# Performance work log

Hardware: AMD Instinct MI355X
Metric: run time of the kernel (lower is better)

## Reference

```python
import jax, jax.numpy as jnp
import numpy as np

N_NODES = 50000
N_EDGES = 800000
IN_CH = 128
HEADS = 4
OUT_CH = 4
N_GRAPHS = 64
NEG_SLOPE = 0.2  # GATv2Conv default leaky_relu slope
EPS = 1e-5       # GraphNorm eps


def _seg_sum(x, seg, n):
    return jax.ops.segment_sum(x, seg, num_segments=n)


def _seg_mean(x, seg, n):
    s = _seg_sum(x, seg, n)
    cnt = _seg_sum(jnp.ones((seg.shape[0],), x.dtype), seg, n)
    return s / jnp.maximum(cnt, 1.0)[:, None]


def gatv2_conv(x, src, dst, n, w_l, w_r, att, bias, heads, out_ch, concat):
    # x: [N, F_in]; src/dst: [E_tot] (self-loops already appended)
    x_l = (x @ w_l).reshape(n, heads, out_ch)
    x_r = (x @ w_r).reshape(n, heads, out_ch)
    m = jax.nn.leaky_relu(x_l[src] + x_r[dst], NEG_SLOPE)   # [E, H, C]
    e = jnp.einsum('ehc,hc->eh', m, att)                    # [E, H]
    # softmax over incoming edges of each destination node
    e_max = jax.ops.segment_max(e, dst, num_segments=n)     # [N, H]
    w = jnp.exp(e - e_max[dst])
    denom = _seg_sum(w, dst, n)                             # [N, H]
    alpha = w / denom[dst]
    out = _seg_sum(alpha[:, :, None] * x_l[src], dst, n)    # [N, H, C]
    out = out.reshape(n, heads * out_ch) if concat else out.mean(axis=1)
    return out + bias


def graph_norm(x, batch, weight, bias, mean_scale, n_graphs):
    mu = _seg_mean(x, batch, n_graphs)                      # [G, C]
    out = x - mu[batch] * mean_scale
    var = _seg_mean(out * out, batch, n_graphs)
    return out / jnp.sqrt(var[batch] + EPS) * weight + bias


def setup_inputs() -> dict:
    key = jax.random.key(0)
    ks = jax.random.split(key, 20)
    H = HEADS
    d = {}
    d['x'] = jax.random.normal(ks[0], (N_NODES, IN_CH), dtype=jnp.float32)
    d['edge_index'] = jax.random.randint(ks[1], (2, N_EDGES), 0, N_NODES, dtype=jnp.int32)
    d['batch'] = jnp.sort(jax.random.randint(ks[2], (N_NODES,), 0, N_GRAPHS, dtype=jnp.int32))
    def glorot(k, shape):
        fan = shape[0] + shape[-1]
        return jax.random.normal(k, shape, dtype=jnp.float32) * np.sqrt(2.0 / fan).astype(np.float32)
    # layer 1: in 128 -> 32 per head, concat -> 128
    d['w_l1'] = glorot(ks[3], (IN_CH, H * 32)); d['w_r1'] = glorot(ks[4], (IN_CH, H * 32))
    d['att1'] = glorot(ks[5], (H, 32)); d['b1'] = jnp.zeros((H * 32,), jnp.float32)
    d['gn1_w'] = jnp.ones((H * 32,), jnp.float32); d['gn1_b'] = jnp.zeros((H * 32,), jnp.float32); d['gn1_s'] = jnp.ones((H * 32,), jnp.float32)
    # layer 2: 128 -> 16 per head, concat -> 64
    d['w_l2'] = glorot(ks[6], (H * 32, H * 16)); d['w_r2'] = glorot(ks[7], (H * 32, H * 16))
    d['att2'] = glorot(ks[8], (H, 16)); d['b2'] = jnp.zeros((H * 16,), jnp.float32)
    d['gn2_w'] = jnp.ones((H * 16,), jnp.float32); d['gn2_b'] = jnp.zeros((H * 16,), jnp.float32); d['gn2_s'] = jnp.ones((H * 16,), jnp.float32)
    # layer 3: 64 -> 8 per head, mean over heads -> 8
    d['w_l3'] = glorot(ks[9], (H * 16, H * 8)); d['w_r3'] = glorot(ks[10], (H * 16, H * 8))
    d['att3'] = glorot(ks[11], (H, 8)); d['b3'] = jnp.zeros((8,), jnp.float32)
    d['gn3_w'] = jnp.ones((8,), jnp.float32); d['gn3_b'] = jnp.zeros((8,), jnp.float32); d['gn3_s'] = jnp.ones((8,), jnp.float32)
    d['lin_w'] = glorot(ks[12], (8, OUT_CH)); d['lin_b'] = jnp.zeros((OUT_CH,), jnp.float32)
    return d


def reference(x, edge_index, batch,
              w_l1, w_r1, att1, b1, gn1_w, gn1_b, gn1_s,
              w_l2, w_r2, att2, b2, gn2_w, gn2_b, gn2_s,
              w_l3, w_r3, att3, b3, gn3_w, gn3_b, gn3_s,
              lin_w, lin_b):
    n = x.shape[0]
    loop = jnp.arange(n, dtype=edge_index.dtype)
    src = jnp.concatenate([edge_index[0], loop])  # add_self_loops=True (PyG default)
    dst = jnp.concatenate([edge_index[1], loop])
    h = gatv2_conv(x, src, dst, n, w_l1, w_r1, att1, b1, HEADS, 32, True)
    h = jax.nn.relu(graph_norm(h, batch, gn1_w, gn1_b, gn1_s, N_GRAPHS))
    h = gatv2_conv(h, src, dst, n, w_l2, w_r2, att2, b2, HEADS, 16, True)
    h = jax.nn.relu(graph_norm(h, batch, gn2_w, gn2_b, gn2_s, N_GRAPHS))
    h = gatv2_conv(h, src, dst, n, w_l3, w_r3, att3, b3, HEADS, 8, False)
    h = jax.nn.relu(graph_norm(h, batch, gn3_w, gn3_b, gn3_s, N_GRAPHS))
    features = _seg_mean(h, batch, N_GRAPHS)  # global_mean_pool -> [G, 8]
    logits = features @ lin_w + lin_b         # [G, OUT_CH]
    return (logits, features)
```

## Files before the change

### kernel.cpp

```cpp
#include <hip/hip_runtime.h>
#include <hip/hip_fp16.h>
#include <math.h>

#define NN 50000
#define NE 800000
#define ET (NE + NN)
#define NG 64
#define H 4
#define NBK 196
#define CH 2048
#define SB ((ET + CH - 1) / CH)
#define GD ((NN + 63) / 64)

typedef _Float16 half8 __attribute__((ext_vector_type(8)));
typedef _Float16 half4 __attribute__((ext_vector_type(4)));
typedef _Float16 hv2 __attribute__((ext_vector_type(2)));
typedef float floatx4 __attribute__((ext_vector_type(4)));


template <int K, int M2>
__device__ __forceinline__ void wprep_fn(int chunk, const float* __restrict__ Wl, const float* __restrict__ Wr,
                                         _Float16* __restrict__ Wfrag) {
    constexpr int MTOT = 2 * M2, NT = MTOT / 16;
    if (chunk >= MTOT * K / 8) return;
    int lane = chunk & 63, tt = chunk >> 6;
    int t = tt % NT, kt = tt / NT;
    int n = t * 16 + (lane & 15);
    int kb = kt * 32 + (lane >> 4) * 8;
    const float* src = (n < M2) ? (Wl + n) : (Wr + (n - M2));
    half8 h;
#pragma unroll
    for (int j = 0; j < 8; ++j) h[j] = (_Float16)src[(size_t)(kb + j) * M2];
    *(half8*)(Wfrag + (size_t)chunk * 8) = h;
}


__global__ __launch_bounds__(256) void k_prep(const float* __restrict__ Wl1, const float* __restrict__ Wr1,
                                              const float* __restrict__ Wl2, const float* __restrict__ Wr2,
                                              const float* __restrict__ Wl3, const float* __restrict__ Wr3,
                                              _Float16* __restrict__ Wf1, _Float16* __restrict__ Wf2,
                                              _Float16* __restrict__ Wf3,
                                              const int* __restrict__ batch, int* __restrict__ bpos,
                                              const int* __restrict__ ei, int* __restrict__ bcnt) {
    int b = blockIdx.x, t = threadIdx.x;
    if (b < 16) { wprep_fn<128, 128>(b * 256 + t, Wl1, Wr1, Wf1); return; }
    if (b < 24) { wprep_fn<128, 64>((b - 16) * 256 + t, Wl2, Wr2, Wf2); return; }
    if (b < 26) { wprep_fn<64, 32>((b - 24) * 256 + t, Wl3, Wr3, Wf3); return; }
    if (b < 26 + NBK) {
        int i = (b - 26) * 256 + t;
        if (i >= NN) return;
        int cur = batch[i];
        int prev = (i == 0) ? -1 : batch[i - 1];
        for (int g = prev + 1; g <= cur; ++g) bpos[g] = i;
        if (i == NN - 1)
            for (int g = cur + 1; g <= NG; ++g) bpos[g] = NN;
        return;
    }
    __shared__ int hist[NBK];
    int b0 = b - 26 - NBK;
    for (int i = t; i < NBK; i += 256) hist[i] = 0;
    __syncthreads();
#pragma unroll
    for (int pass = 0; pass < CH / 256; ++pass) {
        int e = b0 * CH + pass * 256 + t;
        if (e < ET) {
            int d = (e < NE) ? ei[NE + e] : (e - NE);
            atomicAdd(&hist[d >> 8], 1);
        }
    }
    __syncthreads();
    if (t < NBK) bcnt[t * SB + b0] = hist[t];
}


template <typename AT, bool NORM>
__device__ __forceinline__ half8 load_a8(const AT* __restrict__ ap, const float* pa, const float* pb) {
    if constexpr (NORM) {
        half8 raw = *(const half8*)ap;
        half8 h;
#pragma unroll
        for (int j = 0; j < 8; ++j) {
            float y = fmaf((float)raw[j], pa[j], pb[j]);
            h[j] = (_Float16)fmaxf(y, 0.f);
        }
        return h;
    } else if constexpr (__is_same(AT, _Float16)) {
        return *(const half8*)ap;
    } else {
        const float4* p = (const float4*)ap;
        float4 a = p[0], b = p[1];
        half8 h;
        h[0] = (_Float16)a.x; h[1] = (_Float16)a.y; h[2] = (_Float16)a.z; h[3] = (_Float16)a.w;
        h[4] = (_Float16)b.x; h[5] = (_Float16)b.y; h[6] = (_Float16)b.z; h[7] = (_Float16)b.w;
        return h;
    }
}

template <int K, int M2, typename AT, bool NORM>
__device__ __forceinline__ void dualgemm_body(int blk, int tid, const AT* __restrict__ Ain,
                                              const _Float16* __restrict__ Wfrag,
                                              __half* __restrict__ Ol, __half* __restrict__ Or,
                                              const float* __restrict__ gsum, const float* __restrict__ gsq,
                                              const float* __restrict__ gw, const float* __restrict__ gbb,
                                              const float* __restrict__ gms,
                                              const int* __restrict__ bpos, const int* __restrict__ batch) {
    constexpr int MTOT = 2 * M2;
    constexpr int NT = MTOT / 16;
    constexpr int KT = K / 32;
    constexpr int PK = NORM ? K : 1;
    __shared__ float spab[2][8][PK];
    int wid = tid >> 6, lane = tid & 63;
    int q = lane >> 4, l15 = lane & 15;
    int r0 = blk * 64 + wid * 16;
    int arow = min(r0 + l15, NN - 1);
    const AT* ap = Ain + (size_t)arow * K + q * 8;
    const float *pa = nullptr, *pb = nullptr;
    if constexpr (NORM) {
        int rb = blk * 64;
        int g0 = batch[min(rb, NN - 1)];
        int g1 = batch[min(rb + 63, NN - 1)];
        int gspan = min(g1 - g0 + 1, 8);
        for (int i = tid; i < gspan * K; i += 256) {
            int gg = i / K, c = i - gg * K;
            int g = g0 + gg;
            float cg = fmaxf((float)(bpos[g + 1] - bpos[g]), 1.f);
            float mu = gsum[(size_t)g * K + c] / cg;
            float ex2 = gsq[(size_t)g * K + c] / cg;
            float s_ = gms[c];
            float var = ex2 - s_ * (2.f - s_) * mu * mu;
            float a = rsqrtf(var + 1e-5f) * gw[c];
            spab[0][gg][c] = a;
            spab[1][gg][c] = gbb[c] - mu * s_ * a;
        }
        __syncthreads();
        int gg = min(batch[arow] - g0, 7);
        pa = &spab[0][gg][q * 8];
        pb = &spab[1][gg][q * 8];
    }

    floatx4 acc[NT];
#pragma unroll
    for (int t = 0; t < NT; ++t) acc[t] = (floatx4){0.f, 0.f, 0.f, 0.f};

#pragma unroll
    for (int kt = 0; kt < KT; ++kt) {
        half8 a8 = load_a8<AT, NORM>(ap + kt * 32, pa + (NORM ? kt * 32 : 0), pb + (NORM ? kt * 32 : 0));
        const _Float16* wp = Wfrag + ((size_t)(kt * NT) * 64 + lane) * 8;
#pragma unroll
        for (int t = 0; t < NT; ++t) {
            half8 b8 = *(const half8*)(wp + (size_t)t * 64 * 8);
            acc[t] = __builtin_amdgcn_mfma_f32_16x16x32_f16(a8, b8, acc[t], 0, 0, 0);
        }
    }

#pragma unroll
    for (int t = 0; t < NT; ++t) {
        int cn = t * 16 + l15;
#pragma unroll
        for (int reg = 0; reg < 4; ++reg) {
            int r = r0 + q * 4 + reg;
            if (r < NN) {
                if (cn < M2) Ol[(size_t)r * M2 + cn] = __float2half(acc[t][reg]);
                else         Or[(size_t)r * M2 + (cn - M2)] = __float2half(acc[t][reg]);
            }
        }
    }
}

template <int K, int M2>
__global__ __launch_bounds__(256) void k_dualgemm_n(const __half* __restrict__ Ain,
                                                    const _Float16* __restrict__ Wfrag,
                                                    __half* __restrict__ Ol, __half* __restrict__ Or,
                                                    const float* __restrict__ gsum, const float* __restrict__ gsq,
                                                    const float* __restrict__ gw, const float* __restrict__ gbb,
                                                    const float* __restrict__ gms,
                                                    const int* __restrict__ bpos, const int* __restrict__ batch) {
    dualgemm_body<K, M2, _Float16, true>(blockIdx.x, threadIdx.x, (const _Float16*)Ain, Wfrag, Ol, Or,
                                         gsum, gsq, gw, gbb, gms, bpos, batch);
}


__device__ __forceinline__ void bscanA_fn(int b, int t, const int* __restrict__ bcnt,
                                          int* __restrict__ boff, int* __restrict__ tot) {
    __shared__ int lds[256];
    int i0 = 2 * t, i1 = 2 * t + 1;
    int v0 = (i0 < SB) ? bcnt[b * SB + i0] : 0;
    int v1 = (i1 < SB) ? bcnt[b * SB + i1] : 0;
    int pair = v0 + v1;
    lds[t] = pair;
    __syncthreads();
    for (int off = 1; off < 256; off <<= 1) {
        int y = (t >= off) ? lds[t - off] : 0;
        __syncthreads();
        lds[t] += y;
        __syncthreads();
    }
    int excl = lds[t] - pair;
    if (i0 < SB) boff[b * SB + i0] = excl;
    if (i1 < SB) boff[b * SB + i1] = excl + v0;
    if (t == 255) tot[b] = lds[255];
}


__global__ __launch_bounds__(256) void k_gemm1_scan(const float* __restrict__ x, const _Float16* __restrict__ Wf1,
                                                    __half* __restrict__ Ol, __half* __restrict__ Or,
                                                    const int* __restrict__ bcnt, int* __restrict__ boff,
                                                    int* __restrict__ tot) {
    if (blockIdx.x < GD)
        dualgemm_body<128, 128, float, false>(blockIdx.x, threadIdx.x, x, Wf1, Ol, Or,
                                              nullptr, nullptr, nullptr, nullptr, nullptr, nullptr, nullptr);
    else
        bscanA_fn(blockIdx.x - GD, threadIdx.x, bcnt, boff, tot);
}


__device__ __forceinline__ void edge_sd(int e, const int* __restrict__ ei, int& s, int& d) {
    if (e < NE) { s = ei[e]; d = ei[NE + e]; } else { s = e - NE; d = s; }
}

__global__ __launch_bounds__(1024) void k_bscatter(const int* __restrict__ ei, const int* __restrict__ tot,
                                                   const int* __restrict__ boff, unsigned int* __restrict__ ebuf) {
    __shared__ int eb[256];
    __shared__ int cur[NBK];
    int b0 = blockIdx.x, t = threadIdx.x;
    int v = (t < NBK) ? tot[t] : 0;
    if (t < 256) eb[t] = v;
    __syncthreads();
    for (int off = 1; off < 256; off <<= 1) {
        int y = (t >= off && t < 256) ? eb[t - off] : 0;
        __syncthreads();
        if (t < 256) eb[t] += y;
        __syncthreads();
    }
    if (t < NBK) cur[t] = (eb[t] - v) + boff[t * SB + b0];
    __syncthreads();
#pragma unroll
    for (int pass = 0; pass < CH / 1024; ++pass) {
        int e = b0 * CH + pass * 1024 + t;
        if (e < ET) {
            int s, d;
            edge_sd(e, ei, s, d);
            int pos = atomicAdd(&cur[d >> 8], 1);
            ebuf[pos] = ((unsigned)s << 16) | (unsigned)(d & 255);
        }
    }
}


__global__ __launch_bounds__(1024) void k_bsort(const unsigned int* __restrict__ ebuf,
                                                const int* __restrict__ tot,
                                                int* __restrict__ rowptr, unsigned short* __restrict__ colsrc) {
    __shared__ int eb[256];
    __shared__ int sbase;
    __shared__ int cnt2[256];
    __shared__ int sc[256];
    __shared__ int cur2[256];
    int b = blockIdx.x, t = threadIdx.x;
    int v = (t < NBK) ? tot[t] : 0;
    if (t < 256) eb[t] = v;
    __syncthreads();
    for (int off = 1; off < 256; off <<= 1) {
        int y = (t >= off && t < 256) ? eb[t - off] : 0;
        __syncthreads();
        if (t < 256) eb[t] += y;
        __syncthreads();
    }
    if (t == b) sbase = eb[t] - v;
    __syncthreads();
    int base = sbase, n = tot[b];
    if (t < 256) cnt2[t] = 0;
    __syncthreads();
    for (int i = t; i < n; i += 1024) atomicAdd(&cnt2[ebuf[base + i] & 255], 1);
    __syncthreads();
    if (t < 256) sc[t] = cnt2[t];
    __syncthreads();
    for (int off = 1; off < 256; off <<= 1) {
        int y = (t >= off && t < 256) ? sc[t - off] : 0;
        __syncthreads();
        if (t < 256) sc[t] += y;
        __syncthreads();
    }
    if (t < 256) {
        int cv = cnt2[t];
        int excl = sc[t] - cv;
        int d = b * 256 + t;
        if (d < NN) rowptr[d] = base + excl;
        cur2[t] = excl;
    }
    if (b == 0 && t == 0) rowptr[NN] = ET;
    __syncthreads();
    for (int i = t; i < n; i += 1024) {
        unsigned u = ebuf[base + i];
        int pos = atomicAdd(&cur2[u & 255], 1);
        colsrc[base + pos] = (unsigned short)(u >> 16);
    }
}


template <int CP> struct HVec { hv2 h2[CP / 2]; };

template <int CP>
__device__ __forceinline__ HVec<CP> load_hv(const __half* __restrict__ p) {
    HVec<CP> r;
    if constexpr (CP == 16) {
        float4* rp = (float4*)&r;
        rp[0] = ((const float4*)p)[0];
        rp[1] = ((const float4*)p)[1];
    } else if constexpr (CP == 8) {
        float4 t = *(const float4*)p; r = *(HVec<CP>*)&t;
    } else if constexpr (CP == 4) {
        float2 t = *(const float2*)p; r = *(HVec<CP>*)&t;
    } else {
        r.h2[0] = *(const hv2*)p;
    }
    return r;
}

template <int C, int EP, bool CONCAT>
__global__ __launch_bounds__(256) void k_attn(const __half* __restrict__ xl, const __half* __restrict__ xr,
                                              const int* __restrict__ rowptr,
                                              const unsigned short* __restrict__ colsrc,
                                              const float* __restrict__ att, const float* __restrict__ bias,
                                              __half* __restrict__ out) {
    constexpr int CP = C / EP;
    constexpr int LEP = (EP == 4) ? 2 : ((EP == 2) ? 1 : 0);
    int t = blockIdx.x * 256 + threadIdx.x;
    int part = t & (EP - 1);
    int nh = t >> LEP;
    if (nh >= NN * H) return;
    int node = nh >> 2, h = nh & 3;
    int cbase = h * C + part * CP;
    hv2 xrr2[CP / 2], attv2[CP / 2];
    float acc[CP];
    {
        HVec<CP> xrv = load_hv<CP>(xr + (size_t)node * (H * C) + cbase);
        const float* q = att + cbase;
#pragma unroll
        for (int j = 0; j < CP / 2; ++j) {
            xrr2[j] = xrv.h2[j];
            attv2[j] = (hv2){(_Float16)q[2 * j], (_Float16)q[2 * j + 1]};
        }
#pragma unroll
        for (int c = 0; c < CP; ++c) acc[c] = 0.f;
    }
    float denom = 0.f;
    int beg = rowptr[node], end = rowptr[node + 1];

    auto process = [&](const HVec<CP>& xv) {
        float part_s = 0.f;
#pragma unroll
        for (int j = 0; j < CP / 2; ++j) {
            hv2 z = xv.h2[j] + xrr2[j];
            hv2 l = __builtin_elementwise_max(z, z * (_Float16)0.2f);
            part_s = __builtin_amdgcn_fdot2(l, attv2[j], part_s, false);
        }
        float score = part_s;
#pragma unroll
        for (int mask = 1; mask < EP; mask <<= 1) score += __shfl_xor(score, mask, 64);
        float w = __expf(score);
        denom += w;
        const _Float16* xh = (const _Float16*)&xv;
#pragma unroll
        for (int c = 0; c < CP; ++c) acc[c] = fmaf(w, (float)xh[c], acc[c]);
    };

    int idx = beg;
    for (; idx + 8 <= end; idx += 8) {
        int s[8];
#pragma unroll
        for (int u = 0; u < 8; ++u) s[u] = colsrc[idx + u];
        HVec<CP> xv[8];
#pragma unroll
        for (int u = 0; u < 8; ++u) xv[u] = load_hv<CP>(xl + (size_t)s[u] * (H * C) + cbase);
#pragma unroll
        for (int u = 0; u < 8; ++u) process(xv[u]);
    }
    for (; idx + 4 <= end; idx += 4) {
        int s0 = colsrc[idx], s1 = colsrc[idx + 1], s2 = colsrc[idx + 2], s3 = colsrc[idx + 3];
        HVec<CP> xv0 = load_hv<CP>(xl + (size_t)s0 * (H * C) + cbase);
        HVec<CP> xv1 = load_hv<CP>(xl + (size_t)s1 * (H * C) + cbase);
        HVec<CP> xv2 = load_hv<CP>(xl + (size_t)s2 * (H * C) + cbase);
        HVec<CP> xv3 = load_hv<CP>(xl + (size_t)s3 * (H * C) + cbase);
        process(xv0);
        process(xv1);
        process(xv2);
        process(xv3);
    }
    for (; idx < end; ++idx) {
        int s = colsrc[idx];
        HVec<CP> xv = load_hv<CP>(xl + (size_t)s * (H * C) + cbase);
        process(xv);
    }

    float inv = 1.f / denom;
    _Float16* op = (_Float16*)out + (size_t)node * (H * C) + cbase;
    _Float16 hv[CP];
#pragma unroll
    for (int c = 0; c < CP; ++c) {
        float v = acc[c] * inv;
        if (CONCAT) v += bias[cbase + c];
        hv[c] = (_Float16)v;
    }
    if constexpr (CP >= 8) {
#pragma unroll
        for (int j = 0; j < CP / 8; ++j) *(half8*)(op + 8 * j) = *(half8*)(hv + 8 * j);
    } else if constexpr (CP == 4) {
        *(half4*)op = *(half4*)hv;
    } else {
        *(hv2*)op = *(hv2*)hv;
    }
}


template <int LOGC, int SPLIT>
__global__ __launch_bounds__(256) void k_gnred2(const __half* __restrict__ h, const int* __restrict__ bpos,
                                                float* __restrict__ sum, float* __restrict__ sumsq) {
    constexpr int C = 1 << LOGC;
    constexpr int RG = 256 >> LOGC;
    int g = blockIdx.x / SPLIT, s = blockIdx.x % SPLIT;
    int c = threadIdx.x & (C - 1);
    int rg = threadIdx.x >> LOGC;
    int b0 = bpos[g], b1 = bpos[g + 1];
    int n = b1 - b0;
    int seg = (n + SPLIT - 1) / SPLIT;
    int r0 = b0 + s * seg;
    int r1 = min(r0 + seg, b1);
    float sv = 0.f, ssv = 0.f;
    for (int r = r0 + rg; r < r1; r += RG) {
        float x = __half2float(h[(size_t)r * C + c]);
        sv += x; ssv += x * x;
    }
    __shared__ float ls[256], lss[256];
    ls[threadIdx.x] = sv; lss[threadIdx.x] = ssv;
    __syncthreads();
    for (int off = 128; off >= C; off >>= 1) {
        if (threadIdx.x < off) {
            ls[threadIdx.x] += ls[threadIdx.x + off];
            lss[threadIdx.x] += lss[threadIdx.x + off];
        }
        __syncthreads();
    }
    if (threadIdx.x < C) {
        atomicAdd(&sum[g * C + threadIdx.x], ls[threadIdx.x]);
        atomicAdd(&sumsq[g * C + threadIdx.x], lss[threadIdx.x]);
    }
}


template <int SPLIT>
__global__ __launch_bounds__(256) void k_headgn(const __half* __restrict__ tmp, const float* __restrict__ b3,
                                                const int* __restrict__ bpos, float* __restrict__ Af,
                                                float* __restrict__ sum, float* __restrict__ sumsq) {
    constexpr int C = 8, RG = 32;
    int g = blockIdx.x / SPLIT, s = blockIdx.x % SPLIT;
    int c = threadIdx.x & 7;
    int rg = threadIdx.x >> 3;
    int b0 = bpos[g], b1 = bpos[g + 1];
    int n = b1 - b0;
    int seg = (n + SPLIT - 1) / SPLIT;
    int r0 = b0 + s * seg;
    int r1 = min(r0 + seg, b1);
    float bias = b3[c];
    float sv = 0.f, ssv = 0.f;
    for (int r = r0 + rg; r < r1; r += RG) {
        const __half* p = tmp + (size_t)r * 32 + c;
        float v = 0.25f * (__half2float(p[0]) + __half2float(p[8]) +
                           __half2float(p[16]) + __half2float(p[24])) + bias;
        Af[(size_t)r * C + c] = v;
        sv += v; ssv += v * v;
    }
    __shared__ float ls[256], lss[256];
    ls[threadIdx.x] = sv; lss[threadIdx.x] = ssv;
    __syncthreads();
    for (int off = 128; off >= C; off >>= 1) {
        if (threadIdx.x < off) {
            ls[threadIdx.x] += ls[threadIdx.x + off];
            lss[threadIdx.x] += lss[threadIdx.x + off];
        }
        __syncthreads();
    }
    if (threadIdx.x < C) {
        atomicAdd(&sum[g * C + threadIdx.x], ls[threadIdx.x]);
        atomicAdd(&sumsq[g * C + threadIdx.x], lss[threadIdx.x]);
    }
}


__global__ __launch_bounds__(256) void k_gnpool_final(const float* __restrict__ Af, const int* __restrict__ bpos,
                                                      const float* __restrict__ sum, const float* __restrict__ sumsq,
                                                      const float* __restrict__ w,
                                                      const float* __restrict__ b, const float* __restrict__ ms,
                                                      const float* __restrict__ lw, const float* __restrict__ lb,
                                                      float* __restrict__ outp) {
    constexpr int C = 8, RG = 32;
    int g = blockIdx.x;
    int c = threadIdx.x & 7;
    int rg = threadIdx.x >> 3;
    int b0 = bpos[g], b1 = bpos[g + 1];
    int n = b1 - b0;
    float cg = fmaxf((float)n, 1.f);
    float mu = sum[g * C + c] / cg;
    float ex2 = sumsq[g * C + c] / cg;
    float s_ = ms[c];
    float var = ex2 - (2.f * s_ - s_ * s_) * mu * mu;
    float rs = rsqrtf(var + 1e-5f) * w[c];
    float bb = b[c], mus = mu * s_;
    float pv = 0.f;
    for (int r = b0 + rg; r < b1; r += RG) {
        float y = fmaxf((Af[(size_t)r * C + c] - mus) * rs + bb, 0.f);
        pv += y;
    }
    __shared__ float ls[256];
    __shared__ float feat[8];
    ls[threadIdx.x] = pv;
    __syncthreads();
    for (int off = 128; off >= C; off >>= 1) {
        if (threadIdx.x < off) ls[threadIdx.x] += ls[threadIdx.x + off];
        __syncthreads();
    }
    if (threadIdx.x < C) {
        float f = ls[threadIdx.x] / cg;
        feat[threadIdx.x] = f;
        outp[256 + g * 8 + threadIdx.x] = f;
    }
    __syncthreads();
    if (threadIdx.x < 4) {
        float a = lb[threadIdx.x];
#pragma unroll
        for (int cc = 0; cc < 8; ++cc) a += feat[cc] * lw[cc * 4 + threadIdx.x];
        outp[g * 4 + threadIdx.x] = a;
    }
}


extern "C" void kernel_launch(void* const* d_in, const int* in_sizes, int n_in,
                              void* d_out, int out_size, void* d_ws, size_t ws_size,
                              hipStream_t stream) {
    const float* x    = (const float*)d_in[0];
    const int*   ei   = (const int*)d_in[1];
    const int*   batch= (const int*)d_in[2];
    const float *w_l1 = (const float*)d_in[3],  *w_r1 = (const float*)d_in[4];
    const float *att1 = (const float*)d_in[5],  *b1   = (const float*)d_in[6];
    const float *gn1w = (const float*)d_in[7],  *gn1b = (const float*)d_in[8],  *gn1s = (const float*)d_in[9];
    const float *w_l2 = (const float*)d_in[10], *w_r2 = (const float*)d_in[11];
    const float *att2 = (const float*)d_in[12], *b2   = (const float*)d_in[13];
    const float *gn2w = (const float*)d_in[14], *gn2b = (const float*)d_in[15], *gn2s = (const float*)d_in[16];
    const float *w_l3 = (const float*)d_in[17], *w_r3 = (const float*)d_in[18];
    const float *att3 = (const float*)d_in[19], *b3   = (const float*)d_in[20];
    const float *gn3w = (const float*)d_in[21], *gn3b = (const float*)d_in[22], *gn3s = (const float*)d_in[23];
    const float *lw   = (const float*)d_in[24], *lb   = (const float*)d_in[25];

    char* ws = (char*)d_ws;
    size_t off = 0;
    auto alloc = [&](size_t bytes) -> void* {
        void* p = ws + off;
        off += (bytes + 255) & ~(size_t)255;
        return p;
    };
    __half* Ah  = (__half*)alloc((size_t)NN * 128 * 2);
    __half* Bh  = (__half*)alloc((size_t)NN * 128 * 2);
    __half* Chh = (__half*)alloc((size_t)NN * 64 * 2);
    __half* B   = (__half*)alloc((size_t)NN * 128 * 2);
    __half* Cb  = (__half*)alloc((size_t)NN * 64 * 2);
    float*  Af  = (float*)alloc((size_t)NN * 8 * 4);
    _Float16* Wf1 = (_Float16*)alloc((size_t)256 * 128 * 2);
    _Float16* Wf2 = (_Float16*)alloc((size_t)128 * 128 * 2);
    _Float16* Wf3 = (_Float16*)alloc((size_t)64 * 64 * 2);
    int* rowptr = (int*)alloc((size_t)(NN + 1) * 4);
    unsigned short* colsrc = (unsigned short*)alloc((size_t)ET * 2);
    unsigned int* ebuf = (unsigned int*)alloc((size_t)ET * 4);
    int* bcnt   = (int*)alloc((size_t)NBK * SB * 4);
    int* boff   = (int*)alloc((size_t)NBK * SB * 4);
    int* tot    = (int*)alloc((size_t)NBK * 4);
    int* bpos   = (int*)alloc((size_t)(NG + 1) * 4);
    char* zbase = ws + off;
    float* sum1 = (float*)alloc((size_t)NG * 128 * 4);
    float* sq1  = (float*)alloc((size_t)NG * 128 * 4);
    float* sum2 = (float*)alloc((size_t)NG * 64 * 4);
    float* sq2  = (float*)alloc((size_t)NG * 64 * 4);
    float* sum3 = (float*)alloc((size_t)NG * 8 * 4);
    float* sq3  = (float*)alloc((size_t)NG * 8 * 4);
    size_t zbytes = (size_t)((ws + off) - zbase);
    (void)hipMemsetAsync(zbase, 0, zbytes, stream);

    k_prep<<<26 + NBK + SB, 256, 0, stream>>>(w_l1, w_r1, w_l2, w_r2, w_l3, w_r3, Wf1, Wf2, Wf3,
                                              batch, bpos, ei, bcnt);
    k_gemm1_scan<<<GD + NBK, 256, 0, stream>>>(x, Wf1, Ah, B, bcnt, boff, tot);
    k_bscatter<<<SB, 1024, 0, stream>>>(ei, tot, boff, ebuf);
    k_bsort<<<NBK, 1024, 0, stream>>>(ebuf, tot, rowptr, colsrc);

    int gA2ep = (NN * H * 2 + 255) / 256;
    int gA1ep = (NN * H + 255) / 256;

    k_attn<32, 2, true><<<gA2ep, 256, 0, stream>>>(Ah, B, rowptr, colsrc, att1, b1, Bh);
    k_gnred2<7, 8><<<NG * 8, 256, 0, stream>>>(Bh, bpos, sum1, sq1);

    k_dualgemm_n<128, 64><<<GD, 256, 0, stream>>>(Bh, Wf2, Ah, Cb, sum1, sq1, gn1w, gn1b, gn1s, bpos, batch);
    k_attn<16, 2, true><<<gA2ep, 256, 0, stream>>>(Ah, Cb, rowptr, colsrc, att2, b2, Chh);
    k_gnred2<6, 8><<<NG * 8, 256, 0, stream>>>(Chh, bpos, sum2, sq2);

    k_dualgemm_n<64, 32><<<GD, 256, 0, stream>>>(Chh, Wf3, Ah, B, sum2, sq2, gn2w, gn2b, gn2s, bpos, batch);
    k_attn<8, 1, false><<<gA1ep, 256, 0, stream>>>(Ah, B, rowptr, colsrc, att3, nullptr, Bh);
    k_headgn<8><<<NG * 8, 256, 0, stream>>>(Bh, b3, bpos, Af, sum3, sq3);
    k_gnpool_final<<<NG, 256, 0, stream>>>(Af, bpos, sum3, sq3, gn3w, gn3b, gn3s, lw, lb, (float*)d_out);
}
```

Measured before the change: 290.6 us.

## Split layer-1 GEMM across the edge-scatter and edge-sort kernels to overlap work

```diff
diff --git a/kernel.cpp b/kernel.cpp
--- a/kernel.cpp
+++ b/kernel.cpp
@@ -11,6 +11,7 @@
 #define CH 2048
 #define SB ((ET + CH - 1) / CH)
 #define GD ((NN + 63) / 64)
+#define GDH 391
 
 typedef _Float16 half8 __attribute__((ext_vector_type(8)));
 typedef _Float16 half4 __attribute__((ext_vector_type(4)));
@@ -180,9 +181,10 @@
 }
 
 
-__device__ __forceinline__ void bscanA_fn(int b, int t, const int* __restrict__ bcnt,
-                                          int* __restrict__ boff, int* __restrict__ tot) {
+__global__ __launch_bounds__(256) void k_scanA(const int* __restrict__ bcnt,
+                                               int* __restrict__ boff, int* __restrict__ tot) {
     __shared__ int lds[256];
+    int b = blockIdx.x, t = threadIdx.x;
     int i0 = 2 * t, i1 = 2 * t + 1;
     int v0 = (i0 < SB) ? bcnt[b * SB + i0] : 0;
     int v1 = (i1 < SB) ? bcnt[b * SB + i1] : 0;
@@ -202,27 +204,15 @@
 }
 
 
-__global__ __launch_bounds__(256) void k_gemm1_scan(const float* __restrict__ x, const _Float16* __restrict__ Wf1,
-                                                    __half* __restrict__ Ol, __half* __restrict__ Or,
-                                                    const int* __restrict__ bcnt, int* __restrict__ boff,
-                                                    int* __restrict__ tot) {
-    if (blockIdx.x < GD)
-        dualgemm_body<128, 128, float, false>(blockIdx.x, threadIdx.x, x, Wf1, Ol, Or,
-                                              nullptr, nullptr, nullptr, nullptr, nullptr, nullptr, nullptr);
-    else
-        bscanA_fn(blockIdx.x - GD, threadIdx.x, bcnt, boff, tot);
-}
-
-
 __device__ __forceinline__ void edge_sd(int e, const int* __restrict__ ei, int& s, int& d) {
     if (e < NE) { s = ei[e]; d = ei[NE + e]; } else { s = e - NE; d = s; }
 }
 
-__global__ __launch_bounds__(1024) void k_bscatter(const int* __restrict__ ei, const int* __restrict__ tot,
-                                                   const int* __restrict__ boff, unsigned int* __restrict__ ebuf) {
+__device__ __forceinline__ void bscatter_fn(int b0, int t, const int* __restrict__ ei,
+                                            const int* __restrict__ tot, const int* __restrict__ boff,
+                                            unsigned int* __restrict__ ebuf) {
     __shared__ int eb[256];
     __shared__ int cur[NBK];
-    int b0 = blockIdx.x, t = threadIdx.x;
     int v = (t < NBK) ? tot[t] : 0;
     if (t < 256) eb[t] = v;
     __syncthreads();
@@ -235,8 +225,8 @@
     if (t < NBK) cur[t] = (eb[t] - v) + boff[t * SB + b0];
     __syncthreads();
 #pragma unroll
-    for (int pass = 0; pass < CH / 1024; ++pass) {
-        int e = b0 * CH + pass * 1024 + t;
+    for (int pass = 0; pass < CH / 512; ++pass) {
+        int e = b0 * CH + pass * 512 + t;
         if (e < ET) {
             int s, d;
             edge_sd(e, ei, s, d);
@@ -246,16 +236,14 @@
     }
 }
 
-
-__global__ __launch_bounds__(1024) void k_bsort(const unsigned int* __restrict__ ebuf,
-                                                const int* __restrict__ tot,
-                                                int* __restrict__ rowptr, unsigned short* __restrict__ colsrc) {
+__device__ __forceinline__ void bsort_fn(int b, int t, const unsigned int* __restrict__ ebuf,
+                                         const int* __restrict__ tot,
+                                         int* __restrict__ rowptr, unsigned short* __restrict__ colsrc) {
     __shared__ int eb[256];
     __shared__ int sbase;
     __shared__ int cnt2[256];
     __shared__ int sc[256];
     __shared__ int cur2[256];
-    int b = blockIdx.x, t = threadIdx.x;
     int v = (t < NBK) ? tot[t] : 0;
     if (t < 256) eb[t] = v;
     __syncthreads();
@@ -270,7 +258,7 @@
     int base = sbase, n = tot[b];
     if (t < 256) cnt2[t] = 0;
     __syncthreads();
-    for (int i = t; i < n; i += 1024) atomicAdd(&cnt2[ebuf[base + i] & 255], 1);
+    for (int i = t; i < n; i += 512) atomicAdd(&cnt2[ebuf[base + i] & 255], 1);
     __syncthreads();
     if (t < 256) sc[t] = cnt2[t];
     __syncthreads();
@@ -289,11 +277,34 @@
     }
     if (b == 0 && t == 0) rowptr[NN] = ET;
     __syncthreads();
-    for (int i = t; i < n; i += 1024) {
+    for (int i = t; i < n; i += 512) {
         unsigned u = ebuf[base + i];
         int pos = atomicAdd(&cur2[u & 255], 1);
         colsrc[base + pos] = (unsigned short)(u >> 16);
     }
+}
+
+
+__global__ __launch_bounds__(512) void k_bscatter_gemm(const int* __restrict__ ei, const int* __restrict__ tot,
+                                                       const int* __restrict__ boff, unsigned int* __restrict__ ebuf,
+                                                       const float* __restrict__ x, const _Float16* __restrict__ Wf1,
+                                                       __half* __restrict__ Ol, __half* __restrict__ Or) {
+    if (blockIdx.x < SB) { bscatter_fn(blockIdx.x, threadIdx.x, ei, tot, boff, ebuf); return; }
+    if (threadIdx.x >= 256) return;
+    dualgemm_body<128, 128, float, false>(blockIdx.x - SB, threadIdx.x, x, Wf1, Ol, Or,
+                                          nullptr, nullptr, nullptr, nullptr, nullptr, nullptr, nullptr);
+}
+
+
+__global__ __launch_bounds__(512) void k_bsort_gemm(const unsigned int* __restrict__ ebuf,
+                                                    const int* __restrict__ tot,
+                                                    int* __restrict__ rowptr, unsigned short* __restrict__ colsrc,
+                                                    const float* __restrict__ x, const _Float16* __restrict__ Wf1,
+                                                    __half* __restrict__ Ol, __half* __restrict__ Or) {
+    if (blockIdx.x < NBK) { bsort_fn(blockIdx.x, threadIdx.x, ebuf, tot, rowptr, colsrc); return; }
+    if (threadIdx.x >= 256) return;
+    dualgemm_body<128, 128, float, false>(blockIdx.x - NBK + GDH, threadIdx.x, x, Wf1, Ol, Or,
+                                          nullptr, nullptr, nullptr, nullptr, nullptr, nullptr, nullptr);
 }
 
 
@@ -585,9 +596,9 @@
 
     k_prep<<<26 + NBK + SB, 256, 0, stream>>>(w_l1, w_r1, w_l2, w_r2, w_l3, w_r3, Wf1, Wf2, Wf3,
                                               batch, bpos, ei, bcnt);
-    k_gemm1_scan<<<GD + NBK, 256, 0, stream>>>(x, Wf1, Ah, B, bcnt, boff, tot);
-    k_bscatter<<<SB, 1024, 0, stream>>>(ei, tot, boff, ebuf);
-    k_bsort<<<NBK, 1024, 0, stream>>>(ebuf, tot, rowptr, colsrc);
+    k_scanA<<<NBK, 256, 0, stream>>>(bcnt, boff, tot);
+    k_bscatter_gemm<<<SB + GDH, 512, 0, stream>>>(ei, tot, boff, ebuf, x, Wf1, Ah, B);
+    k_bsort_gemm<<<NBK + GDH, 512, 0, stream>>>(ebuf, tot, rowptr, colsrc, x, Wf1, Ah, B);
 
     int gA2ep = (NN * H * 2 + 255) / 256;
     int gA1ep = (NN * H + 255) / 256;
```

Result: no change. 296.0 us (+1.8%).
